# Kernel tuning notes

Hardware: AMD Instinct MI355X
Metric: run time of the kernel (lower is better)

Reference implementation:

```python
import jax, jax.numpy as jnp
import numpy as np


def setup_inputs() -> dict:
    key = jax.random.key(0)
    k1, k2 = jax.random.split(key)
    x = jax.random.normal(k1, (8, 320, 320), dtype=jnp.float32)
    # flow displacements in pixels; scale a bit for realistic motion magnitude
    u = jax.random.normal(k2, (8, 12, 320, 320, 2), dtype=jnp.float32) * 4.0
    return {"x": x, "u": u}


def _bilinear_warp(xf, uf):
    """xf: (P, M, N) images, uf: (P, M, N, 2) flow (u[...,0]=dx cols, u[...,1]=dy rows).
    out(i,j) = bilinear sample of xf at (i + dy, j + dx), zero outside image."""
    P, M, N = xf.shape
    jj = jnp.arange(N, dtype=uf.dtype)            # (N,)
    ii = jnp.arange(M, dtype=uf.dtype)[:, None]   # (M,1)
    sx = jj + uf[..., 0]                          # (P,M,N) sample column
    sy = ii + uf[..., 1]                          # (P,M,N) sample row
    x0 = jnp.floor(sx)
    y0 = jnp.floor(sy)
    wx = sx - x0
    wy = sy - y0
    x0i = x0.astype(jnp.int32)
    y0i = y0.astype(jnp.int32)
    flat = xf.reshape(P, M * N)

    def gather(yi, xi):
        valid = (xi >= 0) & (xi < N) & (yi >= 0) & (yi < M)
        idx = jnp.clip(yi, 0, M - 1) * N + jnp.clip(xi, 0, N - 1)
        v = jnp.take_along_axis(flat, idx.reshape(P, -1), axis=1).reshape(P, M, N)
        return jnp.where(valid, v, jnp.zeros((), xf.dtype))

    v00 = gather(y0i, x0i)
    v01 = gather(y0i, x0i + 1)
    v10 = gather(y0i + 1, x0i)
    v11 = gather(y0i + 1, x0i + 1)
    return (v00 * (1 - wx) * (1 - wy)
            + v01 * wx * (1 - wy)
            + v10 * (1 - wx) * wy
            + v11 * wx * wy)


def reference(x, u):
    F, M, N = u.shape[-4], u.shape[-3], u.shape[-2]
    lead = u.shape[:-4]
    # repeat_interleave(unsqueeze(x,-3), F, dim=-3) == broadcast x across frame dim
    xb = jnp.broadcast_to(jnp.expand_dims(x, -3), lead + (F, M, N)).reshape(-1, M, N)
    uf = u.reshape(-1, M, N, 2)
    out = _bilinear_warp(xb, uf)
    return out.reshape(u.shape[:-1])
```

## Files before the change

kernel.cpp:

```cpp
#include <hip/hip_runtime.h>
#include <hip/hip_fp16.h>

#define PP 8
#define FF 12
#define MM 320
#define NN 320
#define TILE 64
#define HALO 16
#define LW   (TILE + 2 * HALO)
#define PW   49
#define FPB  2

typedef float fvec4 __attribute__((ext_vector_type(4)));

__global__ __launch_bounds__(512, 8) void warp_tile_kernel(
    const float* __restrict__ x,
    const float* __restrict__ u,
    float* __restrict__ out)
{
    __shared__ unsigned int hA[LW * PW];
    __shared__ unsigned int hB[LW * PW];

    int zz = blockIdx.z;
    int p  = zz / (FF / FPB);
    int f0 = (zz % (FF / FPB)) * FPB;
    int i0 = blockIdx.y * TILE;
    int j0 = blockIdx.x * TILE;

    const float* __restrict__ img = x + p * (MM * NN);

    for (int idx = threadIdx.x; idx < LW * (LW / 4); idx += 512) {
        int r  = idx / (LW / 4);
        int c4 = idx - r * (LW / 4);
        int gr = i0 - HALO + r;
        int gc = j0 - HALO + c4 * 4;
        fvec4 v = {0.0f, 0.0f, 0.0f, 0.0f};
        if ((unsigned)gr < MM && (unsigned)gc < NN)
            v = *(const fvec4*)(img + gr * NN + gc);
        __half2 w0 = __floats2half2_rn(v.x, v.y);
        __half2 w1 = __floats2half2_rn(v.z, v.w);
        unsigned int* dst = &hA[r * PW + c4 * 2];
        dst[0] = *(unsigned int*)&w0;
        dst[1] = *(unsigned int*)&w1;
    }
    __syncthreads();

    for (int idx = threadIdx.x; idx < LW * (LW / 2); idx += 512) {
        int r = idx / (LW / 2);
        int c = idx - r * (LW / 2);
        unsigned int a0 = hA[r * PW + c];
        unsigned int a1 = hA[r * PW + c + 1];
        hB[r * PW + c] = __builtin_amdgcn_alignbit(a1, a0, 16);
    }
    __syncthreads();

    int tcol = ((int)threadIdx.x & 15) * 4;
    int row0 = ((int)threadIdx.x >> 4);

#pragma unroll
    for (int ff = 0; ff < FPB; ++ff) {
        int pf = p * FF + (f0 + ff);
        const float* __restrict__ ubase = u + (size_t)pf * (MM * NN * 2);
        float* __restrict__ obase = out + (size_t)pf * (MM * NN);

#pragma unroll
        for (int s = 0; s < 2; ++s) {
            int gi = i0 + row0 + s * 32;
            int gj = j0 + tcol;

            const fvec4* up = (const fvec4*)(ubase + 2 * ((size_t)gi * NN + gj));
            fvec4 ua = up[0];
            fvec4 ub = up[1];
            float dx[4] = {ua.x, ua.z, ub.x, ub.z};
            float dy[4] = {ua.y, ua.w, ub.y, ub.w};

            float res[4];
#pragma unroll
            for (int k = 0; k < 4; ++k) {
                float sx = (float)(gj + k) + dx[k];
                float sy = (float)gi + dy[k];
                float fx0 = floorf(sx);
                float fy0 = floorf(sy);
                float wx = sx - fx0;
                float wy = sy - fy0;
                int x0i = (int)fx0;
                int y0i = (int)fy0;

                int lx = x0i - (j0 - HALO);
                int ly = y0i - (i0 - HALO);

                float v00, v01, v10, v11;
                if ((unsigned)lx < (LW - 1) && (unsigned)ly < (LW - 1)) {
                    const unsigned int* base = (lx & 1) ? hB : hA;
                    int w = ly * PW + (lx >> 1);
                    unsigned int t0 = base[w];
                    unsigned int t1 = base[w + PW];
                    float2 r0 = __half22float2(*(const __half2*)&t0);
                    float2 r1 = __half22float2(*(const __half2*)&t1);
                    v00 = r0.x; v01 = r0.y;
                    v10 = r1.x; v11 = r1.y;
                } else {
                    int xc0 = min(max(x0i,     0), NN - 1);
                    int xc1 = min(max(x0i + 1, 0), NN - 1);
                    int yc0 = min(max(y0i,     0), MM - 1);
                    int yc1 = min(max(y0i + 1, 0), MM - 1);
                    bool vx0 = (x0i >= 0)     & (x0i < NN);
                    bool vx1 = (x0i + 1 >= 0) & (x0i + 1 < NN);
                    bool vy0 = (y0i >= 0)     & (y0i < MM);
                    bool vy1 = (y0i + 1 >= 0) & (y0i + 1 < MM);
                    int r0i = yc0 * NN;
                    int r1i = yc1 * NN;
                    v00 = (vy0 & vx0) ? img[r0i + xc0] : 0.0f;
                    v01 = (vy0 & vx1) ? img[r0i + xc1] : 0.0f;
                    v10 = (vy1 & vx0) ? img[r1i + xc0] : 0.0f;
                    v11 = (vy1 & vx1) ? img[r1i + xc1] : 0.0f;
                }

                float vt = fmaf(wx, v01 - v00, v00);
                float vb = fmaf(wx, v11 - v10, v10);
                res[k] = fmaf(wy, vb - vt, vt);
            }

            fvec4 o = {res[0], res[1], res[2], res[3]};
            __builtin_nontemporal_store(o, (fvec4*)(obase + (size_t)gi * NN + gj));
        }
    }
}

extern "C" void kernel_launch(void* const* d_in, const int* in_sizes, int n_in,
                              void* d_out, int out_size, void* d_ws, size_t ws_size,
                              hipStream_t stream) {
    const float* x = (const float*)d_in[0];
    const float* u = (const float*)d_in[1];
    float* out = (float*)d_out;

    dim3 grid(NN / TILE, MM / TILE, PP * (FF / FPB));
    dim3 block(512);
    warp_tile_kernel<<<grid, block, 0, stream>>>(x, u, out);
}
```

Before: 131.8 us.

## Use fp32 shared tile with smaller 32x32 output tiles per block

Replaces the fp16 packed dual shared-memory tiles (with the shifted copy for odd columns) with a single fp32 shared tile read directly with four scalar loads. The output tile shrinks from 64 to 32, so each thread computes 2 pixels per frame instead of 8, giving more blocks and less LDS per block. It removes the half conversion and the shift pass, and restores full fp32 precision for image values. The cost is a larger halo-to-interior ratio, which means more redundant image loads per output, and fewer independent loads per thread.

```diff
diff --git a/kernel.cpp b/kernel.cpp
--- a/kernel.cpp
+++ b/kernel.cpp
@@ -1,25 +1,24 @@
 #include <hip/hip_runtime.h>
-#include <hip/hip_fp16.h>
 
 #define PP 8
 #define FF 12
 #define MM 320
 #define NN 320
-#define TILE 64
+#define TILE 32
 #define HALO 16
 #define LW   (TILE + 2 * HALO)
-#define PW   49
+#define PW   68
 #define FPB  2
 
 typedef float fvec4 __attribute__((ext_vector_type(4)));
+typedef float fvec2 __attribute__((ext_vector_type(2)));
 
 __global__ __launch_bounds__(512, 8) void warp_tile_kernel(
     const float* __restrict__ x,
     const float* __restrict__ u,
     float* __restrict__ out)
 {
-    __shared__ unsigned int hA[LW * PW];
-    __shared__ unsigned int hB[LW * PW];
+    __shared__ float tile[LW * PW];
 
     int zz = blockIdx.z;
     int p  = zz / (FF / FPB);
@@ -29,33 +28,24 @@
 
     const float* __restrict__ img = x + p * (MM * NN);
 
-    for (int idx = threadIdx.x; idx < LW * (LW / 4); idx += 512) {
-        int r  = idx / (LW / 4);
-        int c4 = idx - r * (LW / 4);
+#pragma unroll
+    for (int it = 0; it < 2; ++it) {
+        int idx = (int)threadIdx.x + it * 512;
+        int r  = idx >> 4;
+        int c4 = idx & 15;
         int gr = i0 - HALO + r;
         int gc = j0 - HALO + c4 * 4;
         fvec4 v = {0.0f, 0.0f, 0.0f, 0.0f};
         if ((unsigned)gr < MM && (unsigned)gc < NN)
             v = *(const fvec4*)(img + gr * NN + gc);
-        __half2 w0 = __floats2half2_rn(v.x, v.y);
-        __half2 w1 = __floats2half2_rn(v.z, v.w);
-        unsigned int* dst = &hA[r * PW + c4 * 2];
-        dst[0] = *(unsigned int*)&w0;
-        dst[1] = *(unsigned int*)&w1;
+        *(fvec4*)&tile[r * PW + c4 * 4] = v;
     }
     __syncthreads();
 
-    for (int idx = threadIdx.x; idx < LW * (LW / 2); idx += 512) {
-        int r = idx / (LW / 2);
-        int c = idx - r * (LW / 2);
-        unsigned int a0 = hA[r * PW + c];
-        unsigned int a1 = hA[r * PW + c + 1];
-        hB[r * PW + c] = __builtin_amdgcn_alignbit(a1, a0, 16);
-    }
-    __syncthreads();
-
-    int tcol = ((int)threadIdx.x & 15) * 4;
+    int tcol = ((int)threadIdx.x & 15) * 2;
     int row0 = ((int)threadIdx.x >> 4);
+    int gi = i0 + row0;
+    int gj = j0 + tcol;
 
 #pragma unroll
     for (int ff = 0; ff < FPB; ++ff) {
@@ -63,67 +53,56 @@
         const float* __restrict__ ubase = u + (size_t)pf * (MM * NN * 2);
         float* __restrict__ obase = out + (size_t)pf * (MM * NN);
 
+        fvec4 ua = *(const fvec4*)(ubase + 2 * ((size_t)gi * NN + gj));
+        float dx[2] = {ua.x, ua.z};
+        float dy[2] = {ua.y, ua.w};
+
+        float res[2];
 #pragma unroll
-        for (int s = 0; s < 2; ++s) {
-            int gi = i0 + row0 + s * 32;
-            int gj = j0 + tcol;
+        for (int k = 0; k < 2; ++k) {
+            float sx = (float)(gj + k) + dx[k];
+            float sy = (float)gi + dy[k];
+            float fx0 = floorf(sx);
+            float fy0 = floorf(sy);
+            float wx = sx - fx0;
+            float wy = sy - fy0;
+            int x0i = (int)fx0;
+            int y0i = (int)fy0;
 
-            const fvec4* up = (const fvec4*)(ubase + 2 * ((size_t)gi * NN + gj));
-            fvec4 ua = up[0];
-            fvec4 ub = up[1];
-            float dx[4] = {ua.x, ua.z, ub.x, ub.z};
-            float dy[4] = {ua.y, ua.w, ub.y, ub.w};
+            int lx = x0i - (j0 - HALO);
+            int ly = y0i - (i0 - HALO);
 
-            float res[4];
-#pragma unroll
-            for (int k = 0; k < 4; ++k) {
-                float sx = (float)(gj + k) + dx[k];
-                float sy = (float)gi + dy[k];
-                float fx0 = floorf(sx);
-                float fy0 = floorf(sy);
-                float wx = sx - fx0;
-                float wy = sy - fy0;
-                int x0i = (int)fx0;
-                int y0i = (int)fy0;
-
-                int lx = x0i - (j0 - HALO);
-                int ly = y0i - (i0 - HALO);
-
-                float v00, v01, v10, v11;
-                if ((unsigned)lx < (LW - 1) && (unsigned)ly < (LW - 1)) {
-                    const unsigned int* base = (lx & 1) ? hB : hA;
-                    int w = ly * PW + (lx >> 1);
-                    unsigned int t0 = base[w];
-                    unsigned int t1 = base[w + PW];
-                    float2 r0 = __half22float2(*(const __half2*)&t0);
-                    float2 r1 = __half22float2(*(const __half2*)&t1);
-                    v00 = r0.x; v01 = r0.y;
-                    v10 = r1.x; v11 = r1.y;
-                } else {
-                    int xc0 = min(max(x0i,     0), NN - 1);
-                    int xc1 = min(max(x0i + 1, 0), NN - 1);
-                    int yc0 = min(max(y0i,     0), MM - 1);
-                    int yc1 = min(max(y0i + 1, 0), MM - 1);
-                    bool vx0 = (x0i >= 0)     & (x0i < NN);
-                    bool vx1 = (x0i + 1 >= 0) & (x0i + 1 < NN);
-                    bool vy0 = (y0i >= 0)     & (y0i < MM);
-                    bool vy1 = (y0i + 1 >= 0) & (y0i + 1 < MM);
-                    int r0i = yc0 * NN;
-                    int r1i = yc1 * NN;
-                    v00 = (vy0 & vx0) ? img[r0i + xc0] : 0.0f;
-                    v01 = (vy0 & vx1) ? img[r0i + xc1] : 0.0f;
-                    v10 = (vy1 & vx0) ? img[r1i + xc0] : 0.0f;
-                    v11 = (vy1 & vx1) ? img[r1i + xc1] : 0.0f;
-                }
-
-                float vt = fmaf(wx, v01 - v00, v00);
-                float vb = fmaf(wx, v11 - v10, v10);
-                res[k] = fmaf(wy, vb - vt, vt);
+            float v00, v01, v10, v11;
+            if (((unsigned)lx < (LW - 1)) & ((unsigned)ly < (LW - 1))) {
+                const float* t = &tile[ly * PW + lx];
+                v00 = t[0];
+                v01 = t[1];
+                v10 = t[PW];
+                v11 = t[PW + 1];
+            } else {
+                int xc0 = min(max(x0i,     0), NN - 1);
+                int xc1 = min(max(x0i + 1, 0), NN - 1);
+                int yc0 = min(max(y0i,     0), MM - 1);
+                int yc1 = min(max(y0i + 1, 0), MM - 1);
+                bool vx0 = (x0i >= 0)     & (x0i < NN);
+                bool vx1 = (x0i + 1 >= 0) & (x0i + 1 < NN);
+                bool vy0 = (y0i >= 0)     & (y0i < MM);
+                bool vy1 = (y0i + 1 >= 0) & (y0i + 1 < MM);
+                int r0i = yc0 * NN;
+                int r1i = yc1 * NN;
+                v00 = (vy0 & vx0) ? img[r0i + xc0] : 0.0f;
+                v01 = (vy0 & vx1) ? img[r0i + xc1] : 0.0f;
+                v10 = (vy1 & vx0) ? img[r1i + xc0] : 0.0f;
+                v11 = (vy1 & vx1) ? img[r1i + xc1] : 0.0f;
             }
 
-            fvec4 o = {res[0], res[1], res[2], res[3]};
-            __builtin_nontemporal_store(o, (fvec4*)(obase + (size_t)gi * NN + gj));
+            float vt = fmaf(wx, v01 - v00, v00);
+            float vb = fmaf(wx, v11 - v10, v10);
+            res[k] = fmaf(wy, vb - vt, vt);
         }
+
+        fvec2 o = {res[0], res[1]};
+        __builtin_nontemporal_store(o, (fvec2*)(obase + (size_t)gi * NN + gj));
     }
 }
 
```

Result: faster. 128.5 us (-2.5%).
